# Optimization experiments

Hardware: AMD Instinct MI355X
Metric: run time of the kernel (lower is better)

Reference implementation:

```python
import jax, jax.numpy as jnp
import numpy as np

IN_C = 128
OUT_C = 128
MEM = 512
HID = MEM // 2  # 256, per ParameterGenerator hidden_channels = memory_size // 2
T = 8          # number of edge types (keys of edge_feas_dict)
N = 500_000


def setup_inputs() -> dict:
    key = jax.random.key(0)
    ks = jax.random.split(key, 16)
    s = 0.02
    inp = {
        "x": jax.random.normal(ks[0], (N, IN_C), dtype=jnp.float32),
        "type_vec": jax.random.randint(ks[1], (N,), 0, T),
        "edge_feas": jax.random.normal(ks[2], (T, MEM), dtype=jnp.float32),
        # weight_generator MLP: Linear(MEM,HID) -> ReLU -> Linear(HID,HID) -> ReLU -> Linear(HID, IN_C*OUT_C)
        "wg_w1": jax.random.normal(ks[3], (MEM, HID), dtype=jnp.float32) * s,
        "wg_b1": jnp.zeros((HID,), dtype=jnp.float32),
        "wg_w2": jax.random.normal(ks[4], (HID, HID), dtype=jnp.float32) * s,
        "wg_b2": jnp.zeros((HID,), dtype=jnp.float32),
        "wg_w3": jax.random.normal(ks[5], (HID, IN_C * OUT_C), dtype=jnp.float32) * s,
        "wg_b3": jnp.zeros((IN_C * OUT_C,), dtype=jnp.float32),
        # bias_generator MLP: Linear(MEM,HID) -> ReLU -> Linear(HID,HID) -> ReLU -> Linear(HID, OUT_C)
        "bg_w1": jax.random.normal(ks[6], (MEM, HID), dtype=jnp.float32) * s,
        "bg_b1": jnp.zeros((HID,), dtype=jnp.float32),
        "bg_w2": jax.random.normal(ks[7], (HID, HID), dtype=jnp.float32) * s,
        "bg_b2": jnp.zeros((HID,), dtype=jnp.float32),
        "bg_w3": jax.random.normal(ks[8], (HID, OUT_C), dtype=jnp.float32) * s,
        "bg_b3": jnp.zeros((OUT_C,), dtype=jnp.float32),
    }
    return inp


def _mlp(m, w1, b1, w2, b2, w3, b3):
    h = jax.nn.relu(m @ w1 + b1)
    h = jax.nn.relu(h @ w2 + b2)
    return h @ w3 + b3


def reference(x, type_vec, edge_feas,
              wg_w1, wg_b1, wg_w2, wg_b2, wg_w3, wg_b3,
              bg_w1, bg_b1, bg_w2, bg_b2, bg_w3, bg_b3):
    # Generate per-type weights [T, IN_C, OUT_C] and biases [T, OUT_C]
    W = _mlp(edge_feas, wg_w1, wg_b1, wg_w2, wg_b2, wg_w3, wg_b3).reshape(T, IN_C, OUT_C)
    B = _mlp(edge_feas, bg_w1, bg_b1, bg_w2, bg_b2, bg_w3, bg_b3)  # [T, OUT_C]
    # Masked per-type linear, scattered back: out[n] = x[n] @ W[type_vec[n]] + B[type_vec[n]]
    out = jnp.zeros((x.shape[0], OUT_C), dtype=x.dtype)
    for t in range(T):  # small fixed set of types
        yt = x @ W[t] + B[t]
        out = jnp.where((type_vec == t)[:, None], yt, out)
    return out
```

## Files before the change

kernel.cpp:

```cpp
#include <hip/hip_runtime.h>
#include <hip/hip_bf16.h>

#define NT 8
#define MEMC 512
#define HID 256
#define C 128

typedef __attribute__((ext_vector_type(8))) short short8;
typedef __attribute__((ext_vector_type(4))) short short4v;
typedef __attribute__((ext_vector_type(4))) float f32x4;

__device__ inline short f2bf(float f) {
    union { __hip_bfloat16 b; short s; } u;
    u.b = __float2bfloat16(f);
    return u.s;
}

__global__ __launch_bounds__(256) void k1_init_genh(
    const float* __restrict__ edge_feas,
    const float* __restrict__ wg_w1, const float* __restrict__ wg_b1,
    const float* __restrict__ wg_w2, const float* __restrict__ wg_b2,
    const float* __restrict__ bg_w1, const float* __restrict__ bg_b1,
    const float* __restrict__ bg_w2, const float* __restrict__ bg_b2,
    int* __restrict__ hist, int* __restrict__ cursor,
    int* __restrict__ idx, int idx_cap,
    float* __restrict__ h_wg, float* __restrict__ h_bg,
    int n_init_blocks)
{
    int b = blockIdx.x, tid = threadIdx.x;
    if (b < n_init_blocks) {
        int pos = b * 1024 + tid * 4;
        if (pos < idx_cap) *(int4*)(idx + pos) = make_int4(-1, -1, -1, -1);
        return;
    }
    if (b == n_init_blocks) {
        if (tid < NT) { hist[tid] = 0; cursor[tid * 16] = 0; }
        return;
    }
    int gb = b - n_init_blocks - 1;
    int t = gb & 7;
    int gen = gb >> 3;
    const float* w1 = gen ? bg_w1 : wg_w1;
    const float* b1 = gen ? bg_b1 : wg_b1;
    const float* w2 = gen ? bg_w2 : wg_w2;
    const float* b2 = gen ? bg_b2 : wg_b2;
    float* hout = gen ? h_bg : h_wg;

    __shared__ float m[MEMC];
    __shared__ float part[4][HID];
    __shared__ float h1[HID];
    m[tid]       = edge_feas[t * MEMC + tid];
    m[tid + 256] = edge_feas[t * MEMC + tid + 256];
    __syncthreads();

    int w = tid >> 6, l = tid & 63;
    {
        float ax = 0.f, ay = 0.f, az = 0.f, aw = 0.f;
        const float* wp = w1 + (size_t)(w * 128) * HID + 4 * l;
        #pragma unroll 8
        for (int k = 0; k < 128; ++k) {
            float4 v = *(const float4*)(wp + (size_t)k * HID);
            float mk = m[w * 128 + k];
            ax += mk * v.x; ay += mk * v.y; az += mk * v.z; aw += mk * v.w;
        }
        *(float4*)&part[w][4 * l] = make_float4(ax, ay, az, aw);
    }
    __syncthreads();
    {
        float s = part[0][tid] + part[1][tid] + part[2][tid] + part[3][tid] + b1[tid];
        h1[tid] = fmaxf(s, 0.f);
    }
    __syncthreads();
    {
        float ax = 0.f, ay = 0.f, az = 0.f, aw = 0.f;
        const float* wp = w2 + (size_t)(w * 64) * HID + 4 * l;
        #pragma unroll 8
        for (int k = 0; k < 64; ++k) {
            float4 v = *(const float4*)(wp + (size_t)k * HID);
            float hk = h1[w * 64 + k];
            ax += hk * v.x; ay += hk * v.y; az += hk * v.z; aw += hk * v.w;
        }
        *(float4*)&part[w][4 * l] = make_float4(ax, ay, az, aw);
    }
    __syncthreads();
    {
        float s = part[0][tid] + part[1][tid] + part[2][tid] + part[3][tid] + b2[tid];
        hout[t * HID + tid] = fmaxf(s, 0.f);
    }
}

__global__ __launch_bounds__(256) void k2_hist_genw(
    const int* __restrict__ type_vec, int N,
    const float* __restrict__ h_wg, const float* __restrict__ h_bg,
    const float* __restrict__ wg_w3, const float* __restrict__ wg_b3,
    const float* __restrict__ bg_w3, const float* __restrict__ bg_b3,
    int* __restrict__ hist, short* __restrict__ Wkn, float* __restrict__ Bias,
    int n_hist_blocks)
{
    int b = blockIdx.x, tid = threadIdx.x;
    __shared__ float sh[2048];
    __shared__ float sp[2048];
    if (b < n_hist_blocks) {
        __shared__ int lh[NT];
        if (tid < NT) lh[tid] = 0;
        __syncthreads();
        int base = b * 1024 + tid;
        #pragma unroll
        for (int i = 0; i < 4; ++i) {
            int n = base + i * 256;
            if (n < N) atomicAdd(&lh[type_vec[n]], 1);
        }
        __syncthreads();
        if (tid < NT) atomicAdd(&hist[tid], lh[tid]);
        return;
    }
    int gb = b - n_hist_blocks;
    if (gb < 256) {
        for (int i = tid; i < 2048; i += 256) sh[i] = h_wg[i];
        __syncthreads();
        int cl = tid & 63, p = tid >> 6;
        int col = gb * 64 + cl;
        float acc[NT];
        #pragma unroll
        for (int t = 0; t < NT; ++t) acc[t] = 0.f;
        const float* wp = wg_w3 + (size_t)(p * 64) * (C * C) + col;
        #pragma unroll 8
        for (int j = 0; j < 64; ++j) {
            float v = wp[(size_t)j * (C * C)];
            #pragma unroll
            for (int t = 0; t < NT; ++t) acc[t] += sh[t * 256 + p * 64 + j] * v;
        }
        #pragma unroll
        for (int t = 0; t < NT; ++t) sp[p * 512 + t * 64 + cl] = acc[t];
        __syncthreads();
        #pragma unroll
        for (int r = 0; r < 2; ++r) {
            int o = tid + 256 * r;
            int t = o >> 6, c2 = o & 63;
            float s = sp[t * 64 + c2] + sp[512 + t * 64 + c2]
                    + sp[1024 + t * 64 + c2] + sp[1536 + t * 64 + c2]
                    + wg_b3[gb * 64 + c2];
            Wkn[t * (C * C) + gb * 64 + c2] = f2bf(s);
        }
        return;
    }
    for (int i = tid; i < 2048; i += 256) sh[i] = h_bg[i];
    __syncthreads();
    int cl = tid & 127, p = tid >> 7;
    float acc[NT];
    #pragma unroll
    for (int t = 0; t < NT; ++t) acc[t] = 0.f;
    const float* wp = bg_w3 + (size_t)(p * 128) * C + cl;
    #pragma unroll 8
    for (int j = 0; j < 128; ++j) {
        float v = wp[(size_t)j * C];
        #pragma unroll
        for (int t = 0; t < NT; ++t) acc[t] += sh[t * 256 + p * 128 + j] * v;
    }
    #pragma unroll
    for (int t = 0; t < NT; ++t) sp[p * 1024 + t * 128 + cl] = acc[t];
    __syncthreads();
    #pragma unroll
    for (int r = 0; r < 4; ++r) {
        int o = tid + 256 * r;
        int t = o >> 7, c2 = o & 127;
        Bias[t * C + c2] = sp[t * 128 + c2] + sp[1024 + t * 128 + c2] + bg_b3[c2];
    }
}

__global__ __launch_bounds__(256) void k4_scatter_transpose(
    const int* __restrict__ type_vec, int N,
    const int* __restrict__ hist, int* __restrict__ cursor,
    int* __restrict__ idx,
    const short* __restrict__ Wkn, short* __restrict__ Wt,
    int n_scatter_blocks)
{
    int b = blockIdx.x, tid = threadIdx.x;
    if (b >= n_scatter_blocks) {
        int t = b - n_scatter_blocks;
        __shared__ short tile[C][C + 8];
        const short* src = Wkn + t * (C * C);
        for (int i = tid; i < C * C; i += 256)
            tile[i >> 7][i & 127] = src[i];
        __syncthreads();
        short* dst = Wt + t * (C * C);
        for (int i = tid; i < C * C; i += 256)
            dst[i] = tile[i & 127][i >> 7];
        return;
    }
    int seg[NT];
    {
        int s = 0;
        #pragma unroll
        for (int t = 0; t < NT; ++t) { seg[t] = s; s += ((hist[t] + 63) >> 6) << 6; }
    }
    int lane = tid & 63;
    int wave = b * 4 + (tid >> 6);
    int start = wave * 1024;
    if (start >= N) return;

    int cnt[NT];
    #pragma unroll
    for (int t = 0; t < NT; ++t) cnt[t] = 0;
    for (int c = 0; c < 16; ++c) {
        int n = start + c * 64 + lane;
        int mt = (n < N) ? type_vec[n] : NT;
        #pragma unroll
        for (int t = 0; t < NT; ++t)
            cnt[t] += __popcll(__ballot(mt == t));
    }
    int base = 0;
    if (lane < NT) base = atomicAdd(&cursor[lane * 16], cnt[lane]);
    int run[NT];
    #pragma unroll
    for (int t = 0; t < NT; ++t) run[t] = seg[t] + __shfl(base, t, 64);
    unsigned long long below = (1ULL << lane) - 1ULL;
    for (int c = 0; c < 16; ++c) {
        int n = start + c * 64 + lane;
        int mt = (n < N) ? type_vec[n] : NT;
        int mypos = 0;
        #pragma unroll
        for (int t = 0; t < NT; ++t) {
            unsigned long long msk = __ballot(mt == t);
            if (mt == t) mypos = run[t] + __popcll(msk & below);
            run[t] += __popcll(msk);
        }
        if (n < N) idx[mypos] = n;
    }
}

__global__ __launch_bounds__(256, 4) void k5_gemm(
    const float* __restrict__ x, const int* __restrict__ idx,
    const short* __restrict__ Wt, const float* __restrict__ Bias,
    const int* __restrict__ hist, float* __restrict__ out)
{
    int tid = threadIdx.x;
    int lane = tid & 63, w = tid >> 6;
    int m16 = lane & 15, quad = lane >> 4;
    int block_base = blockIdx.x * 64;

    int seg[NT + 1];
    {
        int s = 0;
        #pragma unroll
        for (int t = 0; t < NT; ++t) { seg[t] = s; s += ((hist[t] + 63) >> 6) << 6; }
        seg[NT] = s;
    }
    if (block_base >= seg[NT]) return;
    int t = 0;
    #pragma unroll
    for (int i = 1; i < NT; ++i)
        if (block_base >= seg[i]) t = i;

    int row0 = block_base + 16 * w;
    int node_a = idx[row0 + m16];

    short8 af[4];
    {
        const float* xr = x + (size_t)(node_a < 0 ? 0 : node_a) * C + quad * 8;
        #pragma unroll
        for (int kk = 0; kk < 4; ++kk) {
            float4 v0 = *(const float4*)(xr + kk * 32);
            float4 v1 = *(const float4*)(xr + kk * 32 + 4);
            short8 sv;
            sv[0] = f2bf(v0.x); sv[1] = f2bf(v0.y);
            sv[2] = f2bf(v0.z); sv[3] = f2bf(v0.w);
            sv[4] = f2bf(v1.x); sv[5] = f2bf(v1.y);
            sv[6] = f2bf(v1.z); sv[7] = f2bf(v1.w);
            af[kk] = sv;
        }
        if (node_a < 0) {
            #pragma unroll
            for (int kk = 0; kk < 4; ++kk)
                af[kk] = (short8){0, 0, 0, 0, 0, 0, 0, 0};
        }
    }

    f32x4 acc[8];
    #pragma unroll
    for (int i = 0; i < 8; ++i) acc[i] = (f32x4){0.f, 0.f, 0.f, 0.f};

    const short* bw = Wt + t * (C * C) + m16 * C + quad * 8;
    #pragma unroll
    for (int kk = 0; kk < 4; ++kk) {
        #pragma unroll
        for (int ni = 0; ni < 8; ++ni) {
            short8 bf = *(const short8*)(bw + (size_t)ni * 16 * C + kk * 32);
            acc[ni] = __builtin_amdgcn_mfma_f32_16x16x32_bf16(af[kk], bf, acc[ni], 0, 0, 0);
        }
    }

    int node_c[4];
    #pragma unroll
    for (int r = 0; r < 4; ++r) node_c[r] = idx[row0 + quad * 4 + r];

    #pragma unroll
    for (int ni = 0; ni < 8; ++ni) {
        float bv = Bias[t * C + ni * 16 + m16];
        #pragma unroll
        for (int r = 0; r < 4; ++r) {
            if (node_c[r] >= 0)
                out[(size_t)node_c[r] * C + ni * 16 + m16] = acc[ni][r] + bv;
        }
    }
}

extern "C" void kernel_launch(void* const* d_in, const int* in_sizes, int n_in,
                              void* d_out, int out_size, void* d_ws, size_t ws_size,
                              hipStream_t stream)
{
    const float* x         = (const float*)d_in[0];
    const int*   type_vec  = (const int*)d_in[1];
    const float* edge_feas = (const float*)d_in[2];
    const float* wg_w1 = (const float*)d_in[3];
    const float* wg_b1 = (const float*)d_in[4];
    const float* wg_w2 = (const float*)d_in[5];
    const float* wg_b2 = (const float*)d_in[6];
    const float* wg_w3 = (const float*)d_in[7];
    const float* wg_b3 = (const float*)d_in[8];
    const float* bg_w1 = (const float*)d_in[9];
    const float* bg_b1 = (const float*)d_in[10];
    const float* bg_w2 = (const float*)d_in[11];
    const float* bg_b2 = (const float*)d_in[12];
    const float* bg_w3 = (const float*)d_in[13];
    const float* bg_b3 = (const float*)d_in[14];
    float* out = (float*)d_out;
    int N = in_sizes[1];

    char* ws = (char*)d_ws;
    int*   hist   = (int*)(ws + 0);
    int*   cursor = (int*)(ws + 128);
    float* h_wg   = (float*)(ws + 1024);
    float* h_bg   = (float*)(ws + 9216);
    float* Bias   = (float*)(ws + 17408);
    short* Wkn    = (short*)(ws + 21504);
    short* Wt     = (short*)(ws + 283648);
    int*   idx    = (int*)(ws + 545792);

    int nblk64  = (N + 63) / 64;
    int idx_cap = (nblk64 + 8) * 64;
    int n_init  = (idx_cap + 1023) / 1024;
    int n_hist  = (N + 1023) / 1024;
    int n_scat  = (n_hist + 3) / 4;

    k1_init_genh<<<n_init + 17, 256, 0, stream>>>(
        edge_feas, wg_w1, wg_b1, wg_w2, wg_b2, bg_w1, bg_b1, bg_w2, bg_b2,
        hist, cursor, idx, idx_cap, h_wg, h_bg, n_init);

    k2_hist_genw<<<n_hist + 257, 256, 0, stream>>>(
        type_vec, N, h_wg, h_bg, wg_w3, wg_b3, bg_w3, bg_b3,
        hist, Wkn, Bias, n_hist);

    k4_scatter_transpose<<<n_scat + 8, 256, 0, stream>>>(
        type_vec, N, hist, cursor, idx, Wkn, Wt, n_scat);

    k5_gemm<<<nblk64 + 8, 256, 0, stream>>>(x, idx, Wt, Bias, hist, out);
}
```

Baseline: 615.4 us.

## Stage per-type weights in swizzled LDS, 128-row GEMM blocks, fuse transpose

The GEMM kernel now uses 512-thread blocks covering 128 rows. Each block stages the 32KB bf16 weight matrix for its type into LDS with an XOR swizzle, so B fragments come from shared memory instead of repeated global loads. The weight generator writes the transposed layout directly, which removes the separate transpose pass. The histogram uses wave ballots in place of LDS atomics. Segments are padded to 128 rows, which adds padding work and per-block LDS staging cost in exchange for better B reuse.

After: 554.4 us. -9.9%, faster.

```diff
diff --git a/kernel.cpp b/kernel.cpp
--- a/kernel.cpp
+++ b/kernel.cpp
@@ -7,7 +7,6 @@
 #define C 128
 
 typedef __attribute__((ext_vector_type(8))) short short8;
-typedef __attribute__((ext_vector_type(4))) short short4v;
 typedef __attribute__((ext_vector_type(4))) float f32x4;
 
 __device__ inline short f2bf(float f) {
@@ -94,24 +93,27 @@
     const float* __restrict__ h_wg, const float* __restrict__ h_bg,
     const float* __restrict__ wg_w3, const float* __restrict__ wg_b3,
     const float* __restrict__ bg_w3, const float* __restrict__ bg_b3,
-    int* __restrict__ hist, short* __restrict__ Wkn, float* __restrict__ Bias,
+    int* __restrict__ hist, short* __restrict__ Wt, float* __restrict__ Bias,
     int n_hist_blocks)
 {
     int b = blockIdx.x, tid = threadIdx.x;
     __shared__ float sh[2048];
     __shared__ float sp[2048];
     if (b < n_hist_blocks) {
-        __shared__ int lh[NT];
-        if (tid < NT) lh[tid] = 0;
-        __syncthreads();
-        int base = b * 1024 + tid;
-        #pragma unroll
-        for (int i = 0; i < 4; ++i) {
-            int n = base + i * 256;
-            if (n < N) atomicAdd(&lh[type_vec[n]], 1);
-        }
-        __syncthreads();
-        if (tid < NT) atomicAdd(&hist[tid], lh[tid]);
+        int lane = tid & 63, wv = tid >> 6;
+        int start = b * 1024 + wv * 256;
+        int cnt[NT];
+        #pragma unroll
+        for (int t = 0; t < NT; ++t) cnt[t] = 0;
+        #pragma unroll
+        for (int c = 0; c < 4; ++c) {
+            int n = start + c * 64 + lane;
+            int mt = (n < N) ? type_vec[n] : NT;
+            #pragma unroll
+            for (int t = 0; t < NT; ++t)
+                cnt[t] += __popcll(__ballot(mt == t));
+        }
+        if (lane < NT) atomicAdd(&hist[lane], cnt[lane]);
         return;
     }
     int gb = b - n_hist_blocks;
@@ -140,7 +142,8 @@
             float s = sp[t * 64 + c2] + sp[512 + t * 64 + c2]
                     + sp[1024 + t * 64 + c2] + sp[1536 + t * 64 + c2]
                     + wg_b3[gb * 64 + c2];
-            Wkn[t * (C * C) + gb * 64 + c2] = f2bf(s);
+            int flat = gb * 64 + c2;
+            Wt[t * (C * C) + (flat & 127) * C + (flat >> 7)] = f2bf(s);
         }
         return;
     }
@@ -168,31 +171,17 @@
     }
 }
 
-__global__ __launch_bounds__(256) void k4_scatter_transpose(
+__global__ __launch_bounds__(256) void k4_scatter(
     const int* __restrict__ type_vec, int N,
     const int* __restrict__ hist, int* __restrict__ cursor,
-    int* __restrict__ idx,
-    const short* __restrict__ Wkn, short* __restrict__ Wt,
-    int n_scatter_blocks)
+    int* __restrict__ idx)
 {
     int b = blockIdx.x, tid = threadIdx.x;
-    if (b >= n_scatter_blocks) {
-        int t = b - n_scatter_blocks;
-        __shared__ short tile[C][C + 8];
-        const short* src = Wkn + t * (C * C);
-        for (int i = tid; i < C * C; i += 256)
-            tile[i >> 7][i & 127] = src[i];
-        __syncthreads();
-        short* dst = Wt + t * (C * C);
-        for (int i = tid; i < C * C; i += 256)
-            dst[i] = tile[i & 127][i >> 7];
-        return;
-    }
     int seg[NT];
     {
         int s = 0;
         #pragma unroll
-        for (int t = 0; t < NT; ++t) { seg[t] = s; s += ((hist[t] + 63) >> 6) << 6; }
+        for (int t = 0; t < NT; ++t) { seg[t] = s; s += ((hist[t] + 127) >> 7) << 7; }
     }
     int lane = tid & 63;
     int wave = b * 4 + (tid >> 6);
@@ -229,21 +218,22 @@
     }
 }
 
-__global__ __launch_bounds__(256, 4) void k5_gemm(
+__global__ __launch_bounds__(512, 6) void k5_gemm(
     const float* __restrict__ x, const int* __restrict__ idx,
     const short* __restrict__ Wt, const float* __restrict__ Bias,
     const int* __restrict__ hist, float* __restrict__ out)
 {
+    __shared__ short Bs[C * C];
     int tid = threadIdx.x;
     int lane = tid & 63, w = tid >> 6;
     int m16 = lane & 15, quad = lane >> 4;
-    int block_base = blockIdx.x * 64;
+    int block_base = blockIdx.x * 128;
 
     int seg[NT + 1];
     {
         int s = 0;
         #pragma unroll
-        for (int t = 0; t < NT; ++t) { seg[t] = s; s += ((hist[t] + 63) >> 6) << 6; }
+        for (int t = 0; t < NT; ++t) { seg[t] = s; s += ((hist[t] + 127) >> 7) << 7; }
         seg[NT] = s;
     }
     if (block_base >= seg[NT]) return;
@@ -255,38 +245,65 @@
     int row0 = block_base + 16 * w;
     int node_a = idx[row0 + m16];
 
+    short8 bstg[4];
+    {
+        const short* wsrc = Wt + t * (C * C);
+        #pragma unroll
+        for (int i = 0; i < 4; ++i)
+            bstg[i] = *(const short8*)(wsrc + (size_t)(i * 512 + tid) * 8);
+    }
+
+    float4 a0[4], a1[4];
+    {
+        const float* xr = x + (size_t)(node_a < 0 ? 0 : node_a) * C + quad * 8;
+        #pragma unroll
+        for (int kk = 0; kk < 4; ++kk) {
+            a0[kk] = *(const float4*)(xr + kk * 32);
+            a1[kk] = *(const float4*)(xr + kk * 32 + 4);
+        }
+    }
+
+    {
+        #pragma unroll
+        for (int i = 0; i < 4; ++i) {
+            int s = i * 512 + tid;
+            int row = s >> 4, sl = s & 15;
+            *(short8*)((char*)Bs + row * 256 + ((sl ^ (row & 15)) << 4)) = bstg[i];
+        }
+    }
+
+    __syncthreads();
+
     short8 af[4];
-    {
-        const float* xr = x + (size_t)(node_a < 0 ? 0 : node_a) * C + quad * 8;
+    #pragma unroll
+    for (int kk = 0; kk < 4; ++kk) {
+        short8 sv;
+        sv[0] = f2bf(a0[kk].x); sv[1] = f2bf(a0[kk].y);
+        sv[2] = f2bf(a0[kk].z); sv[3] = f2bf(a0[kk].w);
+        sv[4] = f2bf(a1[kk].x); sv[5] = f2bf(a1[kk].y);
+        sv[6] = f2bf(a1[kk].z); sv[7] = f2bf(a1[kk].w);
+        af[kk] = sv;
+    }
+    if (node_a < 0) {
+        #pragma unroll
+        for (int kk = 0; kk < 4; ++kk)
+            af[kk] = (short8){0, 0, 0, 0, 0, 0, 0, 0};
+    }
+
+    f32x4 acc[8];
+    #pragma unroll
+    for (int i = 0; i < 8; ++i) acc[i] = (f32x4){0.f, 0.f, 0.f, 0.f};
+
+    {
+        const char* bbase = (const char*)Bs + m16 * 256;
         #pragma unroll
         for (int kk = 0; kk < 4; ++kk) {
-            float4 v0 = *(const float4*)(xr + kk * 32);
-            float4 v1 = *(const float4*)(xr + kk * 32 + 4);
-            short8 sv;
-            sv[0] = f2bf(v0.x); sv[1] = f2bf(v0.y);
-            sv[2] = f2bf(v0.z); sv[3] = f2bf(v0.w);
-            sv[4] = f2bf(v1.x); sv[5] = f2bf(v1.y);
-            sv[6] = f2bf(v1.z); sv[7] = f2bf(v1.w);
-            af[kk] = sv;
-        }
-        if (node_a < 0) {
+            int cswz = (((kk * 4 + quad) ^ m16) << 4);
             #pragma unroll
-            for (int kk = 0; kk < 4; ++kk)
-                af[kk] = (short8){0, 0, 0, 0, 0, 0, 0, 0};
-        }
-    }
-
-    f32x4 acc[8];
-    #pragma unroll
-    for (int i = 0; i < 8; ++i) acc[i] = (f32x4){0.f, 0.f, 0.f, 0.f};
-
-    const short* bw = Wt + t * (C * C) + m16 * C + quad * 8;
-    #pragma unroll
-    for (int kk = 0; kk < 4; ++kk) {
-        #pragma unroll
-        for (int ni = 0; ni < 8; ++ni) {
-            short8 bf = *(const short8*)(bw + (size_t)ni * 16 * C + kk * 32);
-            acc[ni] = __builtin_amdgcn_mfma_f32_16x16x32_bf16(af[kk], bf, acc[ni], 0, 0, 0);
+            for (int ni = 0; ni < 8; ++ni) {
+                short8 bf = *(const short8*)(bbase + (ni << 12) + cswz);
+                acc[ni] = __builtin_amdgcn_mfma_f32_16x16x32_bf16(af[kk], bf, acc[ni], 0, 0, 0);
+            }
         }
     }
 
@@ -333,12 +350,11 @@
     float* h_wg   = (float*)(ws + 1024);
     float* h_bg   = (float*)(ws + 9216);
     float* Bias   = (float*)(ws + 17408);
-    short* Wkn    = (short*)(ws + 21504);
-    short* Wt     = (short*)(ws + 283648);
-    int*   idx    = (int*)(ws + 545792);
-
-    int nblk64  = (N + 63) / 64;
-    int idx_cap = (nblk64 + 8) * 64;
+    short* Wt     = (short*)(ws + 21504);
+    int*   idx    = (int*)(ws + 283648);
+
+    int nblk128 = (N + 127) / 128;
+    int idx_cap = (nblk128 + 8) * 128;
     int n_init  = (idx_cap + 1023) / 1024;
     int n_hist  = (N + 1023) / 1024;
     int n_scat  = (n_hist + 3) / 4;
@@ -349,10 +365,10 @@
 
     k2_hist_genw<<<n_hist + 257, 256, 0, stream>>>(
         type_vec, N, h_wg, h_bg, wg_w3, wg_b3, bg_w3, bg_b3,
-        hist, Wkn, Bias, n_hist);
-
-    k4_scatter_transpose<<<n_scat + 8, 256, 0, stream>>>(
-        type_vec, N, hist, cursor, idx, Wkn, Wt, n_scat);
-
-    k5_gemm<<<nblk64 + 8, 256, 0, stream>>>(x, idx, Wt, Bias, hist, out);
-}
+        hist, Wt, Bias, n_hist);
+
+    k4_scatter<<<n_scat, 256, 0, stream>>>(
+        type_vec, N, hist, cursor, idx);
+
+    k5_gemm<<<nblk128 + 8, 512, 0, stream>>>(x, idx, Wt, Bias, hist, out);
+}
```
